# Performance work log

Measured on AMD Instinct MI355X. Metric: run time of the kernel, lower is better.

Reference implementation:

```python
import jax, jax.numpy as jnp
import numpy as np

BS, DIM, N, M, O = 2048, 32, 40, 40, 200


def setup_inputs() -> dict:
    key = jax.random.key(0)
    k1, k2, k3 = jax.random.split(key, 3)
    x = jax.random.normal(k1, (BS, DIM, N), dtype=jnp.float32)
    y = jax.random.normal(k2, (BS, DIM, M), dtype=jnp.float32)
    # Linear(n*m -> o), no bias; scale like nn.Linear default-ish init
    W = jax.random.normal(k3, (O, N * M), dtype=jnp.float32) * (1.0 / np.sqrt(N * M))
    return {"x": x, "y": y, "W": W}


def reference(x, y, W):
    # Original math: z[b,d,n,m] = x[b,d,n] * y[b,d,m]; flatten (n,m) -> k; out = z @ W.T
    # Fused form: out[b,d,o] = sum_{n,m} x[b,d,n] * y[b,d,m] * W[o, n*M+m]
    o, nm = W.shape
    Wr = W.reshape(o, x.shape[-1], y.shape[-1])  # [O, N, M]
    return jnp.einsum('bdn,bdm,onm->bdo', x, y, Wr)
```

## Files before the change

### kernel.cpp

```cpp
#include <hip/hip_runtime.h>
#include <hip/hip_fp16.h>

#define OOv   200
#define KKv   1600
#define OPAD  208
#define NSTEPS 50
#define NSUPER 25
#define CHUNK_BYTES 13312
#define HALF0_BYTES 7168
#define XSTR 40
#define YSTR 40

typedef _Float16 half8  __attribute__((ext_vector_type(8)));
typedef _Float16 half2v __attribute__((ext_vector_type(2)));
typedef __attribute__((ext_vector_type(4))) float floatx4;

__global__ void wb_convert_kernel(const float* __restrict__ W,
                                  unsigned short* __restrict__ Wh) {
    int idx = blockIdx.x * 256 + threadIdx.x;
    if (idx >= NSTEPS * OPAD * 32) return;
    int j    = idx & 7;
    int slot = (idx >> 3) % (OPAD * 4);
    int t    = (idx >> 3) / (OPAD * 4);
    int o    = slot >> 2;
    int kgs  = slot & 3;
    int kg   = kgs ^ ((o >> 1) & 3);
    int k    = (4 * (t / 5) + kg) * 40 + 8 * (t % 5) + j;
    float v  = (o < OOv) ? W[o * KKv + k] : 0.0f;
    union { _Float16 h; unsigned short u; } cv; cv.h = (_Float16)v;
    Wh[idx] = cv.u;
}

__global__ __launch_bounds__(256, 2) void cin_mfma_kernel(
        const float* __restrict__ X, const float* __restrict__ Y,
        const unsigned short* __restrict__ Wh, float* __restrict__ Out) {
    __shared__ __align__(16) unsigned char bsm[2 * HALF0_BYTES * 2];
    __shared__ __align__(16) _Float16 xlds[128 * XSTR];
    __shared__ __align__(16) _Float16 ylds[128 * YSTR];

    const int tid     = threadIdx.x;
    const int wave    = tid >> 6;
    const int lane    = tid & 63;
    const int li      = lane & 15;
    const int kg      = lane >> 4;
    const int rowhalf = wave & 1;
    const int colgrp  = wave >> 1;

    const int ch      = blockIdx.x & 1;
    const long blockbase = (long)(blockIdx.x >> 1) * 128;
    const int htiles  = ch ? 6 : 7;
    const int ntiles  = colgrp ? htiles - 4 : 4;
    const int nt      = ch ? (colgrp ? 3 : 3) : (colgrp ? 3 : 4);
    const int cbt     = ch ? (colgrp ? 3 : 0) : (colgrp ? 4 : 0);
    const int half_bytes = ch ? 6144 : 7168;

    const float* xg = X + blockbase * 40;
    const float* yg = Y + blockbase * 40;
    for (int i = tid; i < 1280; i += 256) {
        int r  = i / 10;
        int c4 = (i % 10) * 4;
        floatx4 vx = *(const floatx4*)(xg + i * 4);
        floatx4 vy = *(const floatx4*)(yg + i * 4);
        union { half2v h[2]; unsigned long long u; } px, py;
        px.h[0] = (half2v){(_Float16)vx.x, (_Float16)vx.y};
        px.h[1] = (half2v){(_Float16)vx.z, (_Float16)vx.w};
        py.h[0] = (half2v){(_Float16)vy.x, (_Float16)vy.y};
        py.h[1] = (half2v){(_Float16)vy.z, (_Float16)vy.w};
        *(unsigned long long*)(xlds + r * XSTR + c4) = px.u;
        *(unsigned long long*)(ylds + r * YSTR + c4) = py.u;
    }
    {
        const char* src0 = (const char*)Wh + ch * HALF0_BYTES;
        for (int q = 0; q < 2; ++q) {
            const char* src = src0 + (size_t)q * CHUNK_BYTES;
            unsigned char* dst = bsm + q * HALF0_BYTES;
            for (int u = wave; u * 1024 < half_bytes; u += 4) {
                int off = u * 1024 + lane * 16;
                if (off < half_bytes)
                    __builtin_amdgcn_global_load_lds(
                        (const __attribute__((address_space(1))) unsigned int*)(src + off),
                        (__attribute__((address_space(3))) unsigned int*)(dst + off),
                        16, 0, 0);
            }
        }
    }
    __syncthreads();

    const int rowb = rowhalf * 64 + li;
    half8 yr[4][5];
#pragma unroll
    for (int rt = 0; rt < 4; ++rt) {
        int row = rowb + rt * 16;
#pragma unroll
        for (int grp = 0; grp < 5; ++grp)
            yr[rt][grp] = *(const half8*)(ylds + row * YSTR + grp * 8);
    }

    floatx4 acc[4][4];
#pragma unroll
    for (int rt = 0; rt < 4; ++rt)
#pragma unroll
        for (int ct = 0; ct < 4; ++ct)
            acc[rt][ct] = (floatx4){0.f, 0.f, 0.f, 0.f};

    const int lc0   = cbt * 16 + li;
    const int bfoff = lc0 * 64 + ((kg ^ ((lc0 >> 1) & 3)) * 16);

    for (int mg = 0; mg < 5; ++mg) {
        half2v xs[2][4];
#pragma unroll
        for (int w = 0; w < 2; ++w)
#pragma unroll
            for (int rt = 0; rt < 4; ++rt) {
                _Float16 xv = xlds[(rowb + rt * 16) * XSTR + (2 * mg + w) * 4 + kg];
                xs[w][rt] = (half2v){xv, xv};
            }

#pragma unroll
        for (int ss5 = 0; ss5 < 5; ++ss5) {
            const int sstep = mg * 5 + ss5;
            if (sstep + 1 < NSUPER) {
                const char* src0 = (const char*)Wh + ch * HALF0_BYTES
                                 + (size_t)(2 * sstep + 2) * CHUNK_BYTES;
                unsigned char* dst0 = bsm + ((sstep + 1) & 1) * (2 * HALF0_BYTES);
                for (int q = 0; q < 2; ++q)
                    for (int u = wave; u * 1024 < half_bytes; u += 4) {
                        int off = u * 1024 + lane * 16;
                        if (off < half_bytes)
                            __builtin_amdgcn_global_load_lds(
                                (const __attribute__((address_space(1))) unsigned int*)
                                    (src0 + (size_t)q * CHUNK_BYTES + off),
                                (__attribute__((address_space(3))) unsigned int*)
                                    (dst0 + q * HALF0_BYTES + off),
                                16, 0, 0);
                    }
            }
            const unsigned char* cbuf = bsm + (sstep & 1) * (2 * HALF0_BYTES);

#pragma unroll
            for (int h = 0; h < 2; ++h) {
                const int t  = 2 * sstep + h;
                const int p  = t % 5;
                const int w  = (t / 5) & 1;
                const unsigned char* chunk = cbuf + h * HALF0_BYTES;

                half8 bf[4];
#pragma unroll
                for (int ct = 0; ct < 4; ++ct)
                    if (ct < nt)
                        bf[ct] = *(const half8*)(chunk + bfoff + ct * 1024);

                half8 af[4];
#pragma unroll
                for (int rt = 0; rt < 4; ++rt) {
                    half8 xsp = __builtin_shufflevector(xs[w][rt], xs[w][rt],
                                                        0, 1, 0, 1, 0, 1, 0, 1);
                    af[rt] = xsp * yr[rt][p];
                }

#pragma unroll
                for (int ct = 0; ct < 4; ++ct)
                    if (ct < nt)
#pragma unroll
                        for (int rt = 0; rt < 4; ++rt)
                            acc[rt][ct] = __builtin_amdgcn_mfma_f32_16x16x32_f16(
                                af[rt], bf[ct], acc[rt][ct], 0, 0, 0);
            }
            __syncthreads();
        }
    }

#pragma unroll
    for (int rt = 0; rt < 4; ++rt) {
#pragma unroll
        for (int ct = 0; ct < 4; ++ct) {
            if (ct >= nt) continue;
            int gcol = ch * 112 + (cbt + ct) * 16 + li;
            if (gcol < OOv) {
#pragma unroll
                for (int r4 = 0; r4 < 4; ++r4) {
                    long grow = blockbase + rowhalf * 64 + rt * 16 + kg * 4 + r4;
                    Out[grow * OOv + gcol] = acc[rt][ct][r4];
                }
            }
        }
    }
}

extern "C" void kernel_launch(void* const* d_in, const int* in_sizes, int n_in,
                              void* d_out, int out_size, void* d_ws, size_t ws_size,
                              hipStream_t stream) {
    (void)in_sizes; (void)n_in; (void)out_size; (void)ws_size;
    const float* X = (const float*)d_in[0];
    const float* Y = (const float*)d_in[1];
    const float* W = (const float*)d_in[2];
    float* Out = (float*)d_out;
    unsigned short* Wh = (unsigned short*)d_ws;

    wb_convert_kernel<<<1300, 256, 0, stream>>>(W, Wh);
    cin_mfma_kernel<<<1024, 256, 0, stream>>>(X, Y, Wh, Out);
}
```

Before: 136.5 us.

## Retile CIN kernel to 64-row blocks covering all output columns with 8 waves

Each block now handles 64 rows and all 208 padded output columns using 8 waves (2 row groups × 4 column groups), instead of 128 rows and half the columns with 4 waves. The W tiles are streamed as full 26 KB superchunks double-buffered in LDS, so each block loads the whole W once and the x/y products are no longer recomputed across the two column halves. The trade is fewer rows per block reusing each W load, which means more total W traffic through L2, and more LDS per block, which could limit occupancy.

```diff
diff --git a/kernel.cpp b/kernel.cpp
--- a/kernel.cpp
+++ b/kernel.cpp
@@ -7,7 +7,7 @@
 #define NSTEPS 50
 #define NSUPER 25
 #define CHUNK_BYTES 13312
-#define HALF0_BYTES 7168
+#define SUPER_BYTES 26624
 #define XSTR 40
 #define YSTR 40
 
@@ -31,32 +31,30 @@
     Wh[idx] = cv.u;
 }
 
-__global__ __launch_bounds__(256, 2) void cin_mfma_kernel(
+__global__ __launch_bounds__(512, 4) void cin_mfma_kernel(
         const float* __restrict__ X, const float* __restrict__ Y,
         const unsigned short* __restrict__ Wh, float* __restrict__ Out) {
-    __shared__ __align__(16) unsigned char bsm[2 * HALF0_BYTES * 2];
-    __shared__ __align__(16) _Float16 xlds[128 * XSTR];
-    __shared__ __align__(16) _Float16 ylds[128 * YSTR];
+    __shared__ __align__(16) unsigned char bsm[2 * SUPER_BYTES];
+    __shared__ __align__(16) _Float16 xlds[64 * XSTR];
+    __shared__ __align__(16) _Float16 ylds[64 * YSTR];
 
-    const int tid     = threadIdx.x;
-    const int wave    = tid >> 6;
-    const int lane    = tid & 63;
-    const int li      = lane & 15;
-    const int kg      = lane >> 4;
-    const int rowhalf = wave & 1;
-    const int colgrp  = wave >> 1;
+    const int tid    = threadIdx.x;
+    const int wave   = tid >> 6;
+    const int lane   = tid & 63;
+    const int li     = lane & 15;
+    const int kg     = lane >> 4;
+    const int rowgrp = wave & 1;
+    const int colgrp = wave >> 1;
 
-    const int ch      = blockIdx.x & 1;
-    const long blockbase = (long)(blockIdx.x >> 1) * 128;
-    const int htiles  = ch ? 6 : 7;
-    const int ntiles  = colgrp ? htiles - 4 : 4;
-    const int nt      = ch ? (colgrp ? 3 : 3) : (colgrp ? 3 : 4);
-    const int cbt     = ch ? (colgrp ? 3 : 0) : (colgrp ? 4 : 0);
-    const int half_bytes = ch ? 6144 : 7168;
+    static const int nt_t[4]  = {4, 3, 3, 3};
+    static const int cbt_t[4] = {0, 4, 7, 10};
+    const int nt  = nt_t[colgrp];
+    const int cbt = cbt_t[colgrp];
+    const long blockbase = (long)blockIdx.x * 64;
 
     const float* xg = X + blockbase * 40;
     const float* yg = Y + blockbase * 40;
-    for (int i = tid; i < 1280; i += 256) {
+    for (int i = tid; i < 640; i += 512) {
         int r  = i / 10;
         int c4 = (i % 10) * 4;
         floatx4 vx = *(const floatx4*)(xg + i * 4);
@@ -69,50 +67,41 @@
         *(unsigned long long*)(xlds + r * XSTR + c4) = px.u;
         *(unsigned long long*)(ylds + r * YSTR + c4) = py.u;
     }
-    {
-        const char* src0 = (const char*)Wh + ch * HALF0_BYTES;
-        for (int q = 0; q < 2; ++q) {
-            const char* src = src0 + (size_t)q * CHUNK_BYTES;
-            unsigned char* dst = bsm + q * HALF0_BYTES;
-            for (int u = wave; u * 1024 < half_bytes; u += 4) {
-                int off = u * 1024 + lane * 16;
-                if (off < half_bytes)
-                    __builtin_amdgcn_global_load_lds(
-                        (const __attribute__((address_space(1))) unsigned int*)(src + off),
-                        (__attribute__((address_space(3))) unsigned int*)(dst + off),
-                        16, 0, 0);
-            }
-        }
+    for (int u = wave; u < 26; u += 8) {
+        int off = u * 1024 + lane * 16;
+        __builtin_amdgcn_global_load_lds(
+            (const __attribute__((address_space(1))) unsigned int*)((const char*)Wh + off),
+            (__attribute__((address_space(3))) unsigned int*)(bsm + off),
+            16, 0, 0);
     }
     __syncthreads();
 
-    const int rowb = rowhalf * 64 + li;
-    half8 yr[4][5];
+    half8 yr[2][5];
 #pragma unroll
-    for (int rt = 0; rt < 4; ++rt) {
-        int row = rowb + rt * 16;
+    for (int rt = 0; rt < 2; ++rt) {
+        int row = rowgrp * 32 + rt * 16 + li;
 #pragma unroll
-        for (int grp = 0; grp < 5; ++grp)
-            yr[rt][grp] = *(const half8*)(ylds + row * YSTR + grp * 8);
+        for (int p = 0; p < 5; ++p)
+            yr[rt][p] = *(const half8*)(ylds + row * YSTR + p * 8);
     }
 
-    floatx4 acc[4][4];
+    floatx4 acc[2][4];
 #pragma unroll
-    for (int rt = 0; rt < 4; ++rt)
+    for (int rt = 0; rt < 2; ++rt)
 #pragma unroll
         for (int ct = 0; ct < 4; ++ct)
             acc[rt][ct] = (floatx4){0.f, 0.f, 0.f, 0.f};
 
-    const int lc0   = cbt * 16 + li;
-    const int bfoff = lc0 * 64 + ((kg ^ ((lc0 >> 1) & 3)) * 16);
+    const int bfoff = (cbt * 16 + li) * 64 + ((kg ^ ((li >> 1) & 3)) * 16);
 
     for (int mg = 0; mg < 5; ++mg) {
-        half2v xs[2][4];
+        half2v xs[2][2];
 #pragma unroll
         for (int w = 0; w < 2; ++w)
 #pragma unroll
-            for (int rt = 0; rt < 4; ++rt) {
-                _Float16 xv = xlds[(rowb + rt * 16) * XSTR + (2 * mg + w) * 4 + kg];
+            for (int rt = 0; rt < 2; ++rt) {
+                _Float16 xv = xlds[(rowgrp * 32 + rt * 16 + li) * XSTR
+                                   + (2 * mg + w) * 4 + kg];
                 xs[w][rt] = (half2v){xv, xv};
             }
 
@@ -120,29 +109,24 @@
         for (int ss5 = 0; ss5 < 5; ++ss5) {
             const int sstep = mg * 5 + ss5;
             if (sstep + 1 < NSUPER) {
-                const char* src0 = (const char*)Wh + ch * HALF0_BYTES
-                                 + (size_t)(2 * sstep + 2) * CHUNK_BYTES;
-                unsigned char* dst0 = bsm + ((sstep + 1) & 1) * (2 * HALF0_BYTES);
-                for (int q = 0; q < 2; ++q)
-                    for (int u = wave; u * 1024 < half_bytes; u += 4) {
-                        int off = u * 1024 + lane * 16;
-                        if (off < half_bytes)
-                            __builtin_amdgcn_global_load_lds(
-                                (const __attribute__((address_space(1))) unsigned int*)
-                                    (src0 + (size_t)q * CHUNK_BYTES + off),
-                                (__attribute__((address_space(3))) unsigned int*)
-                                    (dst0 + q * HALF0_BYTES + off),
-                                16, 0, 0);
-                    }
+                const char* src = (const char*)Wh + (size_t)(sstep + 1) * SUPER_BYTES;
+                unsigned char* dst = bsm + ((sstep + 1) & 1) * SUPER_BYTES;
+                for (int u = wave; u < 26; u += 8) {
+                    int off = u * 1024 + lane * 16;
+                    __builtin_amdgcn_global_load_lds(
+                        (const __attribute__((address_space(1))) unsigned int*)(src + off),
+                        (__attribute__((address_space(3))) unsigned int*)(dst + off),
+                        16, 0, 0);
+                }
             }
-            const unsigned char* cbuf = bsm + (sstep & 1) * (2 * HALF0_BYTES);
+            const unsigned char* cbuf = bsm + (sstep & 1) * SUPER_BYTES;
 
 #pragma unroll
             for (int h = 0; h < 2; ++h) {
-                const int t  = 2 * sstep + h;
-                const int p  = t % 5;
-                const int w  = (t / 5) & 1;
-                const unsigned char* chunk = cbuf + h * HALF0_BYTES;
+                const int t = 2 * sstep + h;
+                const int p = t % 5;
+                const int w = (t / 5) & 1;
+                const unsigned char* chunk = cbuf + h * CHUNK_BYTES;
 
                 half8 bf[4];
 #pragma unroll
@@ -150,9 +134,9 @@
                     if (ct < nt)
                         bf[ct] = *(const half8*)(chunk + bfoff + ct * 1024);
 
-                half8 af[4];
+                half8 af[2];
 #pragma unroll
-                for (int rt = 0; rt < 4; ++rt) {
+                for (int rt = 0; rt < 2; ++rt) {
                     half8 xsp = __builtin_shufflevector(xs[w][rt], xs[w][rt],
                                                         0, 1, 0, 1, 0, 1, 0, 1);
                     af[rt] = xsp * yr[rt][p];
@@ -162,7 +146,7 @@
                 for (int ct = 0; ct < 4; ++ct)
                     if (ct < nt)
 #pragma unroll
-                        for (int rt = 0; rt < 4; ++rt)
+                        for (int rt = 0; rt < 2; ++rt)
                             acc[rt][ct] = __builtin_amdgcn_mfma_f32_16x16x32_f16(
                                 af[rt], bf[ct], acc[rt][ct], 0, 0, 0);
             }
@@ -171,15 +155,15 @@
     }
 
 #pragma unroll
-    for (int rt = 0; rt < 4; ++rt) {
+    for (int rt = 0; rt < 2; ++rt) {
 #pragma unroll
         for (int ct = 0; ct < 4; ++ct) {
             if (ct >= nt) continue;
-            int gcol = ch * 112 + (cbt + ct) * 16 + li;
+            int gcol = (cbt + ct) * 16 + li;
             if (gcol < OOv) {
 #pragma unroll
                 for (int r4 = 0; r4 < 4; ++r4) {
-                    long grow = blockbase + rowhalf * 64 + rt * 16 + kg * 4 + r4;
+                    long grow = blockbase + rowgrp * 32 + rt * 16 + kg * 4 + r4;
                     Out[grow * OOv + gcol] = acc[rt][ct][r4];
                 }
             }
@@ -198,5 +182,5 @@
     unsigned short* Wh = (unsigned short*)d_ws;
 
     wb_convert_kernel<<<1300, 256, 0, stream>>>(W, Wh);
-    cin_mfma_kernel<<<1024, 256, 0, stream>>>(X, Y, Wh, Out);
+    cin_mfma_kernel<<<1024, 512, 0, stream>>>(X, Y, Wh, Out);
 }
```

Result: faster. 130.1 us (-4.7%).
